# Performance work log

Hardware: AMD Instinct MI355X
Metric: run time of the kernel (lower is better)

Reference implementation:

```python
import jax, jax.numpy as jnp
import numpy as np

S, D, H = 2048, 2048, 16
HD = D // H  # head dim = 128
LN_EPS = 1e-5


def _ln(x, g, b):
    mu = jnp.mean(x, axis=-1, keepdims=True)
    var = jnp.var(x, axis=-1, keepdims=True)
    return (x - mu) / jnp.sqrt(var + LN_EPS) * g + b


def setup_inputs() -> dict:
    key = jax.random.key(0)
    ks = jax.random.split(key, 8)
    B = 2
    s = 0.02  # weight init scale
    return {
        "x": jax.random.normal(ks[0], (B, S, D), jnp.float32),
        "Wq": jax.random.normal(ks[1], (D, D), jnp.float32) * s,
        "bq": jnp.zeros((D,), jnp.float32),
        "Wk": jax.random.normal(ks[2], (D, D), jnp.float32) * s,
        "bk": jnp.zeros((D,), jnp.float32),
        "Wv": jax.random.normal(ks[3], (D, D), jnp.float32) * s,
        "bv": jnp.zeros((D,), jnp.float32),
        "Wo": jax.random.normal(ks[4], (D, D), jnp.float32) * s,
        "bo": jnp.zeros((D,), jnp.float32),
        "ln1_g": jnp.ones((D,), jnp.float32),
        "ln1_b": jnp.zeros((D,), jnp.float32),
        "ln2_g": jnp.ones((D,), jnp.float32),
        "ln2_b": jnp.zeros((D,), jnp.float32),
        "W1": jax.random.normal(ks[5], (4 * D, D), jnp.float32) * s,
        "b1": jnp.zeros((4 * D,), jnp.float32),
        "W2": jax.random.normal(ks[6], (D, 4 * D), jnp.float32) * s,
        "b2": jnp.zeros((D,), jnp.float32),
    }


def reference(x, Wq, bq, Wk, bk, Wv, bv, Wo, bo,
              ln1_g, ln1_b, ln2_g, ln2_b, W1, b1, W2, b2):
    causal = jnp.tril(jnp.ones((S, S), bool))  # [S, S] lower-triangular mask
    neg = jnp.finfo(x.dtype).min
    inv_sqrt_hd = 1.0 / jnp.sqrt(jnp.asarray(HD, x.dtype))

    def block(xs):  # xs: [S, D] (equinox module is per-sequence; vmapped over batch)
        h = _ln(xs, ln1_g, ln1_b)
        q = (h @ Wq.T + bq).reshape(S, H, HD)
        k = (h @ Wk.T + bk).reshape(S, H, HD)
        v = (h @ Wv.T + bv).reshape(S, H, HD)
        logits = jnp.einsum('shd,Shd->hsS', q, k) * inv_sqrt_hd
        logits = jnp.where(causal, logits, neg)
        attn = jax.nn.softmax(logits, axis=-1)
        o = jnp.einsum('hsS,Shd->shd', attn, v).reshape(S, D)
        h = h + (o @ Wo.T + bo)          # residual of post-ln1 value (as in source)
        h2 = _ln(h, ln2_g, ln2_b)
        m = jax.nn.gelu(h2 @ W1.T + b1) @ W2.T + b2
        return h2 + m                    # residual of post-ln2 value (as in source)

    return jax.vmap(block)(x)
```

## Files before the change

### kernel.cpp

```cpp
#include <hip/hip_runtime.h>
#include <hip/hip_bf16.h>
#include <math.h>

#define DD   2048
#define SS   2048
#define HH   16
#define HDIM 128
#define BB   2
#define MM   4096
#define D4   8192

using bf16x8 = __attribute__((ext_vector_type(8))) short;
using f32x4  = __attribute__((ext_vector_type(4))) float;
using f32x16 = __attribute__((ext_vector_type(16))) float;

__device__ __forceinline__ ushort f2bf(float x) {
  uint u = __builtin_bit_cast(uint, x);
  u += 0x7FFFu + ((u >> 16) & 1u);
  return (ushort)(u >> 16);
}

__device__ __forceinline__ float gelu_f(float v) {
  float u = 0.7978845608028654f * (v + 0.044715f * v * v * v);
  float e = __expf(2.0f * u);
  float th = 1.0f - 2.0f / (e + 1.0f);
  return 0.5f * v * (1.0f + th);
}

__device__ __forceinline__ void gload_lds16(const void* g, void* l) {
  __builtin_amdgcn_global_load_lds(
      (const __attribute__((address_space(1))) void*)g,
      (__attribute__((address_space(3))) void*)l, 16, 0, 0);
}

__global__ __launch_bounds__(256) void cvt_f32_bf16(
    const float* __restrict__ in, ushort* __restrict__ out, int n4) {
  int i = blockIdx.x * 256 + threadIdx.x;
  if (i >= n4) return;
  float4 v = ((const float4*)in)[i];
  ushort4 o;
  o.x = f2bf(v.x); o.y = f2bf(v.y); o.z = f2bf(v.z); o.w = f2bf(v.w);
  ((ushort4*)out)[i] = o;
}

__global__ __launch_bounds__(256) void ln_rows(
    const float* __restrict__ in, const float* __restrict__ gam,
    const float* __restrict__ bet, float* __restrict__ outf,
    ushort* __restrict__ outb) {
  int row = blockIdx.x;
  int t = threadIdx.x;
  const float4* r4 = (const float4*)(in + (size_t)row * DD);
  float4 v0 = r4[t], v1 = r4[t + 256];
  float s = v0.x + v0.y + v0.z + v0.w + v1.x + v1.y + v1.z + v1.w;
  __shared__ float redA[4], redB[4];
  #pragma unroll
  for (int off = 32; off >= 1; off >>= 1) s += __shfl_xor(s, off);
  if ((t & 63) == 0) redA[t >> 6] = s;
  __syncthreads();
  float mean = (redA[0] + redA[1] + redA[2] + redA[3]) * (1.0f / DD);
  float d0 = v0.x - mean, d1 = v0.y - mean, d2 = v0.z - mean, d3 = v0.w - mean;
  float d4 = v1.x - mean, d5 = v1.y - mean, d6 = v1.z - mean, d7 = v1.w - mean;
  float q = d0*d0 + d1*d1 + d2*d2 + d3*d3 + d4*d4 + d5*d5 + d6*d6 + d7*d7;
  #pragma unroll
  for (int off = 32; off >= 1; off >>= 1) q += __shfl_xor(q, off);
  if ((t & 63) == 0) redB[t >> 6] = q;
  __syncthreads();
  float var = (redB[0] + redB[1] + redB[2] + redB[3]) * (1.0f / DD);
  float rstd = rsqrtf(var + 1e-5f);
  const float4* g4 = (const float4*)gam;
  const float4* b4 = (const float4*)bet;
  float4 g0 = g4[t], g1 = g4[t + 256], bb0 = b4[t], bb1 = b4[t + 256];
  float4 y0, y1;
  y0.x = d0 * rstd * g0.x + bb0.x;  y0.y = d1 * rstd * g0.y + bb0.y;
  y0.z = d2 * rstd * g0.z + bb0.z;  y0.w = d3 * rstd * g0.w + bb0.w;
  y1.x = d4 * rstd * g1.x + bb1.x;  y1.y = d5 * rstd * g1.y + bb1.y;
  y1.z = d6 * rstd * g1.z + bb1.z;  y1.w = d7 * rstd * g1.w + bb1.w;
  float4* of4 = (float4*)(outf + (size_t)row * DD);
  of4[t] = y0; of4[t + 256] = y1;
  ushort4 u0, u1;
  u0.x = f2bf(y0.x); u0.y = f2bf(y0.y); u0.z = f2bf(y0.z); u0.w = f2bf(y0.w);
  u1.x = f2bf(y1.x); u1.y = f2bf(y1.y); u1.z = f2bf(y1.z); u1.w = f2bf(y1.w);
  ushort4* ob4 = (ushort4*)(outb + (size_t)row * DD);
  ob4[t] = u0; ob4[t + 256] = u1;
}

template <int OMODE, bool GELU_, bool RES_>
__global__ __launch_bounds__(512, 2) void gemm2(
    const ushort* __restrict__ A, const ushort* __restrict__ Bt,
    const float* __restrict__ bias, const float* __restrict__ res,
    void* __restrict__ Cout, int M, int N, int K) {
  extern __shared__ __align__(16) ushort smem[];
  const int nbm = M >> 8, nbn = N >> 7;
  const int nwg = nbm * nbn;
  int wg = blockIdx.x;
  int wg2 = (wg & 7) * (nwg >> 3) + (wg >> 3);
  int bm = wg2 % nbm, bn = wg2 / nbm;
  int m0 = bm << 8, n0 = bn << 7;
  int t = threadIdx.x, lane = t & 63, w = t >> 6;
  int wm = w >> 2, wn = w & 3;
  int lr = lane & 15, lg = lane >> 4;

  auto stage = [&](int kt, int slot) {
    int k0 = kt << 6;
    ushort* lA = smem + slot * 24576;
    ushort* lB = lA + 16384;
    #pragma unroll
    for (int r = 0; r < 4; r++) {
      int idx = (r << 9) + t;
      int row = idx >> 3, ch = idx & 7;
      gload_lds16(A + (size_t)(m0 + row) * K + k0 + ((ch ^ (row & 7)) << 3),
                  lA + idx * 8);
    }
    #pragma unroll
    for (int r = 0; r < 2; r++) {
      int idx = (r << 9) + t;
      int row = idx >> 3, ch = idx & 7;
      gload_lds16(Bt + (size_t)(n0 + row) * K + k0 + ((ch ^ (row & 7)) << 3),
                  lB + idx * 8);
    }
  };

  f32x4 acc[8][2] = {};
  const int NT = K >> 6;
  stage(0, 0);
  stage(1, 1);
  int slot = 0;
  for (int kt = 0; kt < NT; ++kt) {
    __builtin_amdgcn_sched_barrier(0);
    if (kt + 1 < NT)
      asm volatile("s_waitcnt vmcnt(6) lgkmcnt(0)" ::: "memory");
    else
      asm volatile("s_waitcnt vmcnt(0) lgkmcnt(0)" ::: "memory");
    __builtin_amdgcn_s_barrier();
    __builtin_amdgcn_sched_barrier(0);
    if (kt + 2 < NT) {
      int s2 = slot + 2; if (s2 >= 3) s2 -= 3;
      stage(kt + 2, s2);
    }
    const ushort* lA = smem + slot * 24576;
    const ushort* lB = lA + 16384;
    bf16x8 af[8][2], bfr[2][2];
    #pragma unroll
    for (int mi = 0; mi < 8; mi++) {
      int row = wm * 128 + mi * 16 + lr;
      #pragma unroll
      for (int ks = 0; ks < 2; ks++)
        af[mi][ks] = *(const bf16x8*)
            &lA[row * 64 + (((ks * 4 + lg) ^ (row & 7)) << 3)];
    }
    #pragma unroll
    for (int ni = 0; ni < 2; ni++) {
      int row = wn * 32 + ni * 16 + lr;
      #pragma unroll
      for (int ks = 0; ks < 2; ks++)
        bfr[ni][ks] = *(const bf16x8*)
            &lB[row * 64 + (((ks * 4 + lg) ^ (row & 7)) << 3)];
    }
    __builtin_amdgcn_s_setprio(1);
    #pragma unroll
    for (int ks = 0; ks < 2; ks++)
      #pragma unroll
      for (int mi = 0; mi < 8; mi++)
        #pragma unroll
        for (int ni = 0; ni < 2; ni++)
          acc[mi][ni] = __builtin_amdgcn_mfma_f32_16x16x32_bf16(
              af[mi][ks], bfr[ni][ks], acc[mi][ni], 0, 0, 0);
    __builtin_amdgcn_s_setprio(0);
    slot = (slot + 1 == 3) ? 0 : slot + 1;
  }

  float bv[2];
  #pragma unroll
  for (int ni = 0; ni < 2; ni++) bv[ni] = bias[n0 + wn * 32 + ni * 16 + lr];

  if (OMODE == 2) {
    #pragma unroll
    for (int mi = 0; mi < 8; mi++) {
      int mg = m0 + wm * 128 + mi * 16 + lg * 4;
      int bb_ = mg >> 11, sb = mg & 2047;
      #pragma unroll
      for (int ni = 0; ni < 2; ni++) {
        int n = n0 + wn * 32 + ni * 16 + lr;
        ushort4 u4;
        u4.x = f2bf(acc[mi][ni][0] + bv[ni]);
        u4.y = f2bf(acc[mi][ni][1] + bv[ni]);
        u4.z = f2bf(acc[mi][ni][2] + bv[ni]);
        u4.w = f2bf(acc[mi][ni][3] + bv[ni]);
        size_t idx = ((size_t)((bb_ << 4) | (n >> 7)) * 128 + (n & 127)) * 2048
                     + sb;
        *(ushort4*)&((ushort*)Cout)[idx] = u4;
      }
    }
    return;
  }

  #pragma unroll
  for (int mi = 0; mi < 8; mi++) {
    #pragma unroll
    for (int r = 0; r < 4; r++) {
      int m = m0 + wm * 128 + mi * 16 + lg * 4 + r;
      #pragma unroll
      for (int ni = 0; ni < 2; ni++) {
        int n = n0 + wn * 32 + ni * 16 + lr;
        size_t idx = (size_t)m * N + n;
        float v = acc[mi][ni][r] + bv[ni];
        if (RES_) v += res[idx];
        if (GELU_) v = gelu_f(v);
        if (OMODE == 1) ((ushort*)Cout)[idx] = f2bf(v);
        else            ((float*)Cout)[idx] = v;
      }
    }
  }
}

__global__ __launch_bounds__(256) void attn_fwd(
    const ushort* __restrict__ qb, const ushort* __restrict__ kb,
    const ushort* __restrict__ vTb, ushort* __restrict__ ob) {
  __shared__ ushort Ks[64 * 128];
  __shared__ ushort Vs[128 * 64];
  __shared__ ushort Ps[4][32 * 64];

  int blk = blockIdx.x;
  int i15 = blk & 15;
  int qt = (blk & 256) ? i15 : 15 - i15;
  int bh = blk >> 4;
  int b = bh >> 4, h = bh & 15;
  int q0 = qt << 7;
  int t = threadIdx.x, lane = t & 63, w = t >> 6;
  int l31 = lane & 31, hi = lane >> 5;
  const size_t base = (size_t)b * SS * DD + (size_t)h * HDIM;
  const ushort* qp = qb + base;
  const ushort* kp = kb + base;
  const ushort* vp = vTb + (size_t)bh * HDIM * SS;
  int wq0 = q0 + w * 32;
  int qg = wq0 + l31;

  bf16x8 qf[8];
  #pragma unroll
  for (int kk = 0; kk < 8; kk++)
    qf[kk] = *(const bf16x8*)(qp + (size_t)qg * DD + kk * 16 + hi * 8);

  f32x16 o[4] = {};
  float mu = -1e30f, lrow = 0.f;
  const float csc = 0.08838834764831845f * 1.4426950408889634f;

  int nIter = 2 * qt + 2;
  for (int it = 0; it < nIter; ++it) {
    int kv0 = it * 64;
    #pragma unroll
    for (int ii = 0; ii < 4; ii++) {
      int chunk = ii * 256 + t;
      int row = chunk >> 4, cc = chunk & 15;
      gload_lds16(kp + (size_t)(kv0 + row) * DD + ((cc ^ (row & 15)) << 3),
                  &Ks[chunk * 8]);
    }
    #pragma unroll
    for (int ii = 0; ii < 4; ii++) {
      int chunk = ii * 256 + t;
      int row = chunk >> 3, cc = chunk & 7;
      gload_lds16(vp + (size_t)row * SS + kv0 + ((cc ^ (row & 7)) << 3),
                  &Vs[chunk * 8]);
    }
    __syncthreads();

    if (kv0 <= wq0 + 31) {
      f32x16 s2[2] = {};
      #pragma unroll
      for (int nt = 0; nt < 2; nt++) {
        int row = nt * 32 + l31;
        #pragma unroll
        for (int kk = 0; kk < 8; kk++) {
          bf16x8 kf = *(const bf16x8*)
              &Ks[row * 128 + (((kk * 2 + hi) ^ (row & 15)) << 3)];
          s2[nt] = __builtin_amdgcn_mfma_f32_32x32x16_bf16(kf, qf[kk], s2[nt],
                                                           0, 0, 0);
        }
      }
      float mx = -3e38f;
      #pragma unroll
      for (int nt = 0; nt < 2; nt++) {
        #pragma unroll
        for (int r = 0; r < 16; r++) {
          int kvl = nt * 32 + (r & 3) + 8 * (r >> 2) + 4 * hi;
          float u = (kv0 + kvl > qg) ? -3e38f : s2[nt][r] * csc;
          s2[nt][r] = u;
          mx = fmaxf(mx, u);
        }
      }
      mx = fmaxf(mx, __shfl_xor(mx, 32));
      float mnew = fmaxf(mu, mx);
      float fr = exp2f(mu - mnew);
      mu = mnew;
      float sum = 0.f;
      #pragma unroll
      for (int nt = 0; nt < 2; nt++)
        #pragma unroll
        for (int r = 0; r < 16; r++) {
          float p = exp2f(s2[nt][r] - mnew);
          s2[nt][r] = p;
          sum += p;
        }
      sum += __shfl_xor(sum, 32);
      lrow = lrow * fr + sum;
      #pragma unroll
      for (int dt = 0; dt < 4; dt++)
        #pragma unroll
        for (int r = 0; r < 16; r++) o[dt][r] *= fr;
      #pragma unroll
      for (int nt = 0; nt < 2; nt++) {
        #pragma unroll
        for (int g2 = 0; g2 < 4; g2++) {
          ushort4 u4;
          u4.x = f2bf(s2[nt][g2 * 4 + 0]);
          u4.y = f2bf(s2[nt][g2 * 4 + 1]);
          u4.z = f2bf(s2[nt][g2 * 4 + 2]);
          u4.w = f2bf(s2[nt][g2 * 4 + 3]);
          int cp = (nt * 4 + g2) ^ (l31 & 7);
          *(ushort4*)&Ps[w][l31 * 64 + cp * 8 + hi * 4] = u4;
        }
      }
      asm volatile("s_waitcnt lgkmcnt(0)" ::: "memory");
      #pragma unroll
      for (int kk = 0; kk < 4; kk++) {
        bf16x8 pf = *(const bf16x8*)
            &Ps[w][l31 * 64 + (((kk * 2 + hi) ^ (l31 & 7)) << 3)];
        #pragma unroll
        for (int dt = 0; dt < 4; dt++) {
          int drow = dt * 32 + l31;
          bf16x8 vf = *(const bf16x8*)
              &Vs[drow * 64 + (((kk * 2 + hi) ^ (drow & 7)) << 3)];
          o[dt] = __builtin_amdgcn_mfma_f32_32x32x16_bf16(vf, pf, o[dt],
                                                          0, 0, 0);
        }
      }
    }
    __syncthreads();
  }

  float inv = 1.0f / lrow;
  #pragma unroll
  for (int dt = 0; dt < 4; dt++) {
    #pragma unroll
    for (int g2 = 0; g2 < 4; g2++) {
      ushort4 u4;
      u4.x = f2bf(o[dt][g2 * 4 + 0] * inv);
      u4.y = f2bf(o[dt][g2 * 4 + 1] * inv);
      u4.z = f2bf(o[dt][g2 * 4 + 2] * inv);
      u4.w = f2bf(o[dt][g2 * 4 + 3] * inv);
      int d = dt * 32 + 8 * g2 + 4 * hi;
      *(ushort4*)&ob[base + (size_t)qg * DD + d] = u4;
    }
  }
}

extern "C" void kernel_launch(void* const* d_in, const int* in_sizes, int n_in,
                              void* d_out, int out_size, void* d_ws,
                              size_t ws_size, hipStream_t stream) {
  const float* x    = (const float*)d_in[0];
  const float* Wq   = (const float*)d_in[1];
  const float* bq   = (const float*)d_in[2];
  const float* Wk   = (const float*)d_in[3];
  const float* bk   = (const float*)d_in[4];
  const float* Wv   = (const float*)d_in[5];
  const float* bv   = (const float*)d_in[6];
  const float* Wo   = (const float*)d_in[7];
  const float* bo   = (const float*)d_in[8];
  const float* ln1g = (const float*)d_in[9];
  const float* ln1b = (const float*)d_in[10];
  const float* ln2g = (const float*)d_in[11];
  const float* ln2b = (const float*)d_in[12];
  const float* W1   = (const float*)d_in[13];
  const float* b1   = (const float*)d_in[14];
  const float* W2   = (const float*)d_in[15];
  const float* b2   = (const float*)d_in[16];

  char* ws = (char*)d_ws;
  ushort* Wqb = (ushort*)(ws);
  ushort* Wkb = Wqb + (size_t)DD * DD;
  ushort* Wvb = Wkb + (size_t)DD * DD;
  ushort* Wob = Wvb + (size_t)DD * DD;
  ushort* W1b = (ushort*)(ws);
  ushort* W2b = W1b + (size_t)D4 * DD;
  ushort* qbf = (ushort*)(ws + 67108864);
  ushort* kbf = qbf + (size_t)MM * DD;
  ushort* vTt = kbf + (size_t)MM * DD;
  ushort* aob = vTt + (size_t)MM * DD;
  ushort* gb  = (ushort*)(ws + 67108864);
  float* hf  = (float*)(ws + 134217728);
  float* h2f = hf;
  ushort* hb  = (ushort*)(ws + 167772160);
  ushort* h2b = hb;
  float* h2in = (float*)(ws + 184549376);
  float* out  = (float*)d_out;

  const int LDSB = 147456;
  hipFuncSetAttribute((const void*)gemm2<1, false, false>,
                      hipFuncAttributeMaxDynamicSharedMemorySize, LDSB);
  hipFuncSetAttribute((const void*)gemm2<2, false, false>,
                      hipFuncAttributeMaxDynamicSharedMemorySize, LDSB);
  hipFuncSetAttribute((const void*)gemm2<0, false, true>,
                      hipFuncAttributeMaxDynamicSharedMemorySize, LDSB);
  hipFuncSetAttribute((const void*)gemm2<1, true, false>,
                      hipFuncAttributeMaxDynamicSharedMemorySize, LDSB);

  dim3 blk(256);
  dim3 gblk(512);
  cvt_f32_bf16<<<DD * DD / 4 / 256, blk, 0, stream>>>(Wq, Wqb, DD * DD / 4);
  cvt_f32_bf16<<<DD * DD / 4 / 256, blk, 0, stream>>>(Wk, Wkb, DD * DD / 4);
  cvt_f32_bf16<<<DD * DD / 4 / 256, blk, 0, stream>>>(Wv, Wvb, DD * DD / 4);
  cvt_f32_bf16<<<DD * DD / 4 / 256, blk, 0, stream>>>(Wo, Wob, DD * DD / 4);
  ln_rows<<<MM, blk, 0, stream>>>(x, ln1g, ln1b, hf, hb);
  gemm2<1, false, false><<<256, gblk, LDSB, stream>>>(hb, Wqb, bq, nullptr, qbf, MM, DD, DD);
  gemm2<1, false, false><<<256, gblk, LDSB, stream>>>(hb, Wkb, bk, nullptr, kbf, MM, DD, DD);
  gemm2<2, false, false><<<256, gblk, LDSB, stream>>>(hb, Wvb, bv, nullptr, vTt, MM, DD, DD);
  attn_fwd<<<512, blk, 0, stream>>>(qbf, kbf, vTt, aob);
  gemm2<0, false, true><<<256, gblk, LDSB, stream>>>(aob, Wob, bo, hf, h2in, MM, DD, DD);
  ln_rows<<<MM, blk, 0, stream>>>(h2in, ln2g, ln2b, h2f, h2b);
  cvt_f32_bf16<<<D4 * DD / 4 / 256, blk, 0, stream>>>(W1, W1b, D4 * DD / 4);
  cvt_f32_bf16<<<D4 * DD / 4 / 256, blk, 0, stream>>>(W2, W2b, D4 * DD / 4);
  gemm2<1, true, false><<<1024, gblk, LDSB, stream>>>(h2b, W1b, b1, nullptr, gb, MM, D4, DD);
  gemm2<0, false, true><<<256, gblk, LDSB, stream>>>(gb, W2b, b2, h2f, out, MM, DD, D4);
}
```

Before: 673.8 us.

## Rework GEMM to 4-wave 256x128 tiles, fuse QKV, split-K the MLP down-projection

Replaces the 512-thread GEMM with a 256-thread variant that uses BK=32 tiles without the XOR swizzle and a larger per-wave N footprint. It fuses the Q, K and V projections into one launch over a concatenated weight, and splits the W2 GEMM into two K halves. The halves are written as bf16 partials and summed by a new elementwise kernel along with the bias and residual. The aims are fewer launches, better occupancy on the down projection and lower LDS use. The risks are LDS bank conflicts from dropping the swizzle and precision loss from rounding the partial sums to bf16.

```diff
diff --git a/kernel.cpp b/kernel.cpp
--- a/kernel.cpp
+++ b/kernel.cpp
@@ -18,6 +18,9 @@
   uint u = __builtin_bit_cast(uint, x);
   u += 0x7FFFu + ((u >> 16) & 1u);
   return (ushort)(u >> 16);
+}
+__device__ __forceinline__ float bf2f(ushort u) {
+  return __builtin_bit_cast(float, (uint)u << 16);
 }
 
 __device__ __forceinline__ float gelu_f(float v) {
@@ -85,123 +88,157 @@
 }
 
 template <int OMODE, bool GELU_, bool RES_>
-__global__ __launch_bounds__(512, 2) void gemm2(
+__global__ __launch_bounds__(256, 2) void gemm3(
     const ushort* __restrict__ A, const ushort* __restrict__ Bt,
-    const float* __restrict__ bias, const float* __restrict__ res,
-    void* __restrict__ Cout, int M, int N, int K) {
+    const float* __restrict__ pb0, const float* __restrict__ pb1,
+    const float* __restrict__ pb2, const float* __restrict__ res,
+    void* __restrict__ Cout, int M, int N, int Kfull, int Kloc) {
   extern __shared__ __align__(16) ushort smem[];
   const int nbm = M >> 8, nbn = N >> 7;
   const int nwg = nbm * nbn;
-  int wg = blockIdx.x;
-  int wg2 = (wg & 7) * (nwg >> 3) + (wg >> 3);
+  int wgr = blockIdx.x;
+  int ksl = 0;
+  if (OMODE == 4) { ksl = wgr / nwg; wgr = wgr % nwg; }
+  int wg2 = (wgr & 7) * (nwg >> 3) + (wgr >> 3);
   int bm = wg2 % nbm, bn = wg2 / nbm;
   int m0 = bm << 8, n0 = bn << 7;
+  int kbase = ksl * Kloc;
   int t = threadIdx.x, lane = t & 63, w = t >> 6;
-  int wm = w >> 2, wn = w & 3;
+  int wm = w >> 1, wn = w & 1;
   int lr = lane & 15, lg = lane >> 4;
 
   auto stage = [&](int kt, int slot) {
-    int k0 = kt << 6;
-    ushort* lA = smem + slot * 24576;
-    ushort* lB = lA + 16384;
+    int k0 = kbase + (kt << 5);
+    ushort* lA = smem + slot * 12288;
+    ushort* lB = lA + 8192;
     #pragma unroll
     for (int r = 0; r < 4; r++) {
-      int idx = (r << 9) + t;
-      int row = idx >> 3, ch = idx & 7;
-      gload_lds16(A + (size_t)(m0 + row) * K + k0 + ((ch ^ (row & 7)) << 3),
-                  lA + idx * 8);
+      int idx = (r << 8) + t;
+      int row = idx >> 2, c = idx & 3;
+      gload_lds16(A + (size_t)(m0 + row) * Kfull + k0 + c * 8, lA + idx * 8);
     }
     #pragma unroll
     for (int r = 0; r < 2; r++) {
-      int idx = (r << 9) + t;
-      int row = idx >> 3, ch = idx & 7;
-      gload_lds16(Bt + (size_t)(n0 + row) * K + k0 + ((ch ^ (row & 7)) << 3),
-                  lB + idx * 8);
+      int idx = (r << 8) + t;
+      int row = idx >> 2, c = idx & 3;
+      gload_lds16(Bt + (size_t)(n0 + row) * Kfull + k0 + c * 8, lB + idx * 8);
     }
   };
 
-  f32x4 acc[8][2] = {};
-  const int NT = K >> 6;
+  f32x4 acc[8][4] = {};
+  const int NT = Kloc >> 5;
   stage(0, 0);
   stage(1, 1);
   int slot = 0;
   for (int kt = 0; kt < NT; ++kt) {
     __builtin_amdgcn_sched_barrier(0);
     if (kt + 1 < NT)
-      asm volatile("s_waitcnt vmcnt(6) lgkmcnt(0)" ::: "memory");
+      asm volatile("s_waitcnt vmcnt(6)" ::: "memory");
     else
-      asm volatile("s_waitcnt vmcnt(0) lgkmcnt(0)" ::: "memory");
+      asm volatile("s_waitcnt vmcnt(0)" ::: "memory");
     __builtin_amdgcn_s_barrier();
     __builtin_amdgcn_sched_barrier(0);
     if (kt + 2 < NT) {
       int s2 = slot + 2; if (s2 >= 3) s2 -= 3;
       stage(kt + 2, s2);
     }
-    const ushort* lA = smem + slot * 24576;
-    const ushort* lB = lA + 16384;
-    bf16x8 af[8][2], bfr[2][2];
+    const ushort* lA = smem + slot * 12288;
+    const ushort* lB = lA + 8192;
+    bf16x8 afr[8], bfr[4];
     #pragma unroll
     for (int mi = 0; mi < 8; mi++) {
       int row = wm * 128 + mi * 16 + lr;
-      #pragma unroll
-      for (int ks = 0; ks < 2; ks++)
-        af[mi][ks] = *(const bf16x8*)
-            &lA[row * 64 + (((ks * 4 + lg) ^ (row & 7)) << 3)];
-    }
-    #pragma unroll
-    for (int ni = 0; ni < 2; ni++) {
-      int row = wn * 32 + ni * 16 + lr;
-      #pragma unroll
-      for (int ks = 0; ks < 2; ks++)
-        bfr[ni][ks] = *(const bf16x8*)
-            &lB[row * 64 + (((ks * 4 + lg) ^ (row & 7)) << 3)];
+      afr[mi] = *(const bf16x8*)&lA[row * 32 + lg * 8];
+    }
+    #pragma unroll
+    for (int ni = 0; ni < 4; ni++) {
+      int row = wn * 64 + ni * 16 + lr;
+      bfr[ni] = *(const bf16x8*)&lB[row * 32 + lg * 8];
     }
     __builtin_amdgcn_s_setprio(1);
     #pragma unroll
-    for (int ks = 0; ks < 2; ks++)
-      #pragma unroll
-      for (int mi = 0; mi < 8; mi++)
-        #pragma unroll
-        for (int ni = 0; ni < 2; ni++)
-          acc[mi][ni] = __builtin_amdgcn_mfma_f32_16x16x32_bf16(
-              af[mi][ks], bfr[ni][ks], acc[mi][ni], 0, 0, 0);
+    for (int mi = 0; mi < 8; mi++)
+      #pragma unroll
+      for (int ni = 0; ni < 4; ni++)
+        acc[mi][ni] = __builtin_amdgcn_mfma_f32_16x16x32_bf16(
+            afr[mi], bfr[ni], acc[mi][ni], 0, 0, 0);
     __builtin_amdgcn_s_setprio(0);
     slot = (slot + 1 == 3) ? 0 : slot + 1;
   }
 
-  float bv[2];
-  #pragma unroll
-  for (int ni = 0; ni < 2; ni++) bv[ni] = bias[n0 + wn * 32 + ni * 16 + lr];
-
-  if (OMODE == 2) {
+  if (OMODE == 4) {
+    ushort* Cp = (ushort*)Cout + (size_t)ksl * M * N;
     #pragma unroll
     for (int mi = 0; mi < 8; mi++) {
-      int mg = m0 + wm * 128 + mi * 16 + lg * 4;
-      int bb_ = mg >> 11, sb = mg & 2047;
-      #pragma unroll
-      for (int ni = 0; ni < 2; ni++) {
-        int n = n0 + wn * 32 + ni * 16 + lr;
-        ushort4 u4;
-        u4.x = f2bf(acc[mi][ni][0] + bv[ni]);
-        u4.y = f2bf(acc[mi][ni][1] + bv[ni]);
-        u4.z = f2bf(acc[mi][ni][2] + bv[ni]);
-        u4.w = f2bf(acc[mi][ni][3] + bv[ni]);
-        size_t idx = ((size_t)((bb_ << 4) | (n >> 7)) * 128 + (n & 127)) * 2048
-                     + sb;
-        *(ushort4*)&((ushort*)Cout)[idx] = u4;
+      #pragma unroll
+      for (int r = 0; r < 4; r++) {
+        int m = m0 + wm * 128 + mi * 16 + lg * 4 + r;
+        #pragma unroll
+        for (int ni = 0; ni < 4; ni++) {
+          int n = n0 + wn * 64 + ni * 16 + lr;
+          Cp[(size_t)m * N + n] = f2bf(acc[mi][ni][r]);
+        }
       }
     }
     return;
   }
 
+  if (OMODE == 3) {
+    int seg = n0 >> 11;
+    const float* pb = (seg == 0) ? pb0 : (seg == 1) ? pb1 : pb2;
+    int c0 = n0 - (seg << 11);
+    float bv[4];
+    #pragma unroll
+    for (int ni = 0; ni < 4; ni++) bv[ni] = pb[c0 + wn * 64 + ni * 16 + lr];
+    if (seg < 2) {
+      ushort* dst = (ushort*)((seg == 0) ? pb1 : pb2, nullptr);
+      ushort* q_or_k = (ushort*)Cout + (size_t)seg * MM * DD;
+      #pragma unroll
+      for (int mi = 0; mi < 8; mi++) {
+        #pragma unroll
+        for (int r = 0; r < 4; r++) {
+          int m = m0 + wm * 128 + mi * 16 + lg * 4 + r;
+          #pragma unroll
+          for (int ni = 0; ni < 4; ni++) {
+            int col = c0 + wn * 64 + ni * 16 + lr;
+            q_or_k[(size_t)m * DD + col] = f2bf(acc[mi][ni][r] + bv[ni]);
+          }
+        }
+      }
+    } else {
+      ushort* vT = (ushort*)Cout + (size_t)2 * MM * DD;
+      #pragma unroll
+      for (int mi = 0; mi < 8; mi++) {
+        int mg = m0 + wm * 128 + mi * 16 + lg * 4;
+        int bb_ = mg >> 11, sb = mg & 2047;
+        #pragma unroll
+        for (int ni = 0; ni < 4; ni++) {
+          int col = c0 + wn * 64 + ni * 16 + lr;
+          int h = col >> 7, d = col & 127;
+          ushort4 u4;
+          u4.x = f2bf(acc[mi][ni][0] + bv[ni]);
+          u4.y = f2bf(acc[mi][ni][1] + bv[ni]);
+          u4.z = f2bf(acc[mi][ni][2] + bv[ni]);
+          u4.w = f2bf(acc[mi][ni][3] + bv[ni]);
+          size_t idx = ((size_t)(bb_ * 16 + h) * 128 + d) * 2048 + sb;
+          *(ushort4*)&vT[idx] = u4;
+        }
+      }
+    }
+    return;
+  }
+
+  float bv[4];
+  #pragma unroll
+  for (int ni = 0; ni < 4; ni++) bv[ni] = pb0[n0 + wn * 64 + ni * 16 + lr];
   #pragma unroll
   for (int mi = 0; mi < 8; mi++) {
     #pragma unroll
     for (int r = 0; r < 4; r++) {
       int m = m0 + wm * 128 + mi * 16 + lg * 4 + r;
       #pragma unroll
-      for (int ni = 0; ni < 2; ni++) {
-        int n = n0 + wn * 32 + ni * 16 + lr;
+      for (int ni = 0; ni < 4; ni++) {
+        int n = n0 + wn * 64 + ni * 16 + lr;
         size_t idx = (size_t)m * N + n;
         float v = acc[mi][ni][r] + bv[ni];
         if (RES_) v += res[idx];
@@ -211,6 +248,22 @@
       }
     }
   }
+}
+
+__global__ __launch_bounds__(256) void mlp_fin(
+    const ushort* __restrict__ p, const float* __restrict__ res,
+    const float* __restrict__ b2, float* __restrict__ out) {
+  int i4 = blockIdx.x * 256 + threadIdx.x;
+  ushort4 a = ((const ushort4*)p)[i4];
+  ushort4 b = ((const ushort4*)(p + (size_t)MM * DD))[i4];
+  float4 r = ((const float4*)res)[i4];
+  float4 g = ((const float4*)b2)[i4 & 511];
+  float4 o;
+  o.x = bf2f(a.x) + bf2f(b.x) + r.x + g.x;
+  o.y = bf2f(a.y) + bf2f(b.y) + r.y + g.y;
+  o.z = bf2f(a.z) + bf2f(b.z) + r.z + g.z;
+  o.w = bf2f(a.w) + bf2f(b.w) + r.w + g.w;
+  ((float4*)out)[i4] = o;
 }
 
 __global__ __launch_bounds__(256) void attn_fwd(
@@ -375,13 +428,12 @@
   const float* b2   = (const float*)d_in[16];
 
   char* ws = (char*)d_ws;
-  ushort* Wqb = (ushort*)(ws);
-  ushort* Wkb = Wqb + (size_t)DD * DD;
-  ushort* Wvb = Wkb + (size_t)DD * DD;
-  ushort* Wob = Wvb + (size_t)DD * DD;
+  ushort* Wqkvb = (ushort*)(ws);
+  ushort* Wob   = Wqkvb + (size_t)3 * DD * DD;
   ushort* W1b = (ushort*)(ws);
   ushort* W2b = W1b + (size_t)D4 * DD;
-  ushort* qbf = (ushort*)(ws + 67108864);
+  ushort* qkvb = (ushort*)(ws + 67108864);
+  ushort* qbf = qkvb;
   ushort* kbf = qbf + (size_t)MM * DD;
   ushort* vTt = kbf + (size_t)MM * DD;
   ushort* aob = vTt + (size_t)MM * DD;
@@ -391,33 +443,36 @@
   ushort* hb  = (ushort*)(ws + 167772160);
   ushort* h2b = hb;
   float* h2in = (float*)(ws + 184549376);
+  ushort* pmlp = (ushort*)(ws + 184549376);
   float* out  = (float*)d_out;
 
-  const int LDSB = 147456;
-  hipFuncSetAttribute((const void*)gemm2<1, false, false>,
+  const int LDSB = 73728;
+  hipFuncSetAttribute((const void*)gemm3<3, false, false>,
                       hipFuncAttributeMaxDynamicSharedMemorySize, LDSB);
-  hipFuncSetAttribute((const void*)gemm2<2, false, false>,
+  hipFuncSetAttribute((const void*)gemm3<0, false, true>,
                       hipFuncAttributeMaxDynamicSharedMemorySize, LDSB);
-  hipFuncSetAttribute((const void*)gemm2<0, false, true>,
+  hipFuncSetAttribute((const void*)gemm3<1, true, false>,
                       hipFuncAttributeMaxDynamicSharedMemorySize, LDSB);
-  hipFuncSetAttribute((const void*)gemm2<1, true, false>,
+  hipFuncSetAttribute((const void*)gemm3<4, false, false>,
                       hipFuncAttributeMaxDynamicSharedMemorySize, LDSB);
 
   dim3 blk(256);
-  dim3 gblk(512);
-  cvt_f32_bf16<<<DD * DD / 4 / 256, blk, 0, stream>>>(Wq, Wqb, DD * DD / 4);
-  cvt_f32_bf16<<<DD * DD / 4 / 256, blk, 0, stream>>>(Wk, Wkb, DD * DD / 4);
-  cvt_f32_bf16<<<DD * DD / 4 / 256, blk, 0, stream>>>(Wv, Wvb, DD * DD / 4);
-  cvt_f32_bf16<<<DD * DD / 4 / 256, blk, 0, stream>>>(Wo, Wob, DD * DD / 4);
+  cvt_f32_bf16<<<DD * DD / 1024, blk, 0, stream>>>(Wq, Wqkvb, DD * DD / 4);
+  cvt_f32_bf16<<<DD * DD / 1024, blk, 0, stream>>>(Wk, Wqkvb + (size_t)DD * DD, DD * DD / 4);
+  cvt_f32_bf16<<<DD * DD / 1024, blk, 0, stream>>>(Wv, Wqkvb + (size_t)2 * DD * DD, DD * DD / 4);
+  cvt_f32_bf16<<<DD * DD / 1024, blk, 0, stream>>>(Wo, Wob, DD * DD / 4);
   ln_rows<<<MM, blk, 0, stream>>>(x, ln1g, ln1b, hf, hb);
-  gemm2<1, false, false><<<256, gblk, LDSB, stream>>>(hb, Wqb, bq, nullptr, qbf, MM, DD, DD);
-  gemm2<1, false, false><<<256, gblk, LDSB, stream>>>(hb, Wkb, bk, nullptr, kbf, MM, DD, DD);
-  gemm2<2, false, false><<<256, gblk, LDSB, stream>>>(hb, Wvb, bv, nullptr, vTt, MM, DD, DD);
+  gemm3<3, false, false><<<768, blk, LDSB, stream>>>(
+      hb, Wqkvb, bq, bk, bv, nullptr, qkvb, MM, 3 * DD, DD, DD);
   attn_fwd<<<512, blk, 0, stream>>>(qbf, kbf, vTt, aob);
-  gemm2<0, false, true><<<256, gblk, LDSB, stream>>>(aob, Wob, bo, hf, h2in, MM, DD, DD);
+  gemm3<0, false, true><<<256, blk, LDSB, stream>>>(
+      aob, Wob, bo, bo, bo, hf, h2in, MM, DD, DD, DD);
   ln_rows<<<MM, blk, 0, stream>>>(h2in, ln2g, ln2b, h2f, h2b);
-  cvt_f32_bf16<<<D4 * DD / 4 / 256, blk, 0, stream>>>(W1, W1b, D4 * DD / 4);
-  cvt_f32_bf16<<<D4 * DD / 4 / 256, blk, 0, stream>>>(W2, W2b, D4 * DD / 4);
-  gemm2<1, true, false><<<1024, gblk, LDSB, stream>>>(h2b, W1b, b1, nullptr, gb, MM, D4, DD);
-  gemm2<0, false, true><<<256, gblk, LDSB, stream>>>(gb, W2b, b2, h2f, out, MM, DD, D4);
-}
+  cvt_f32_bf16<<<D4 * DD / 1024, blk, 0, stream>>>(W1, W1b, D4 * DD / 4);
+  cvt_f32_bf16<<<D4 * DD / 1024, blk, 0, stream>>>(W2, W2b, D4 * DD / 4);
+  gemm3<1, true, false><<<1024, blk, LDSB, stream>>>(
+      h2b, W1b, b1, b1, b1, nullptr, gb, MM, D4, DD, DD);
+  gemm3<4, false, false><<<512, blk, LDSB, stream>>>(
+      gb, W2b, b2, b2, b2, nullptr, pmlp, MM, DD, D4, D4 / 2);
+  mlp_fin<<<MM * DD / 1024, blk, 0, stream>>>(pmlp, h2f, b2, out);
+}
```

New measurement: 710.1 us. 1.05x slower.
